# Optimization experiments

Measured on AMD Instinct MI355X. Metric: run time of the kernel, lower is better.

Reference implementation:

```python
import jax, jax.numpy as jnp
import numpy as np

B, S, H = 2, 2048, 2048
NH, NG = 16, 4           # attention heads, query groups
HD = H // NH             # head_dim = 128
HPG = NH // NG           # heads per group = 4


def setup_inputs() -> dict:
    key = jax.random.key(0)
    ks = jax.random.split(key, 8)
    s = 0.02
    return {
        "hidden_states": jax.random.normal(ks[0], (B, S, H), dtype=jnp.float32),
        "attention_mask": jnp.ones((B, S), dtype=jnp.int32),
        "Wq": jax.random.normal(ks[1], (H, H), dtype=jnp.float32) * s,
        "bq": jnp.zeros((H,), dtype=jnp.float32),
        "Wk": jax.random.normal(ks[2], (HD * NG, H), dtype=jnp.float32) * s,
        "bk": jnp.zeros((HD * NG,), dtype=jnp.float32),
        "Wv": jax.random.normal(ks[3], (HD * NG, H), dtype=jnp.float32) * s,
        "bv": jnp.zeros((HD * NG,), dtype=jnp.float32),
    }


def reference(hidden_states, attention_mask, Wq, bq, Wk, bk, Wv, bv):
    b, s, _ = hidden_states.shape
    scale = 1.0 / np.sqrt(HD).astype(np.float32)
    # projections (torch Linear: x @ W.T + b)
    q = hidden_states @ Wq.T + bq                      # [b,s,H]
    k = hidden_states @ Wk.T + bk                      # [b,s,NG*HD]
    v = hidden_states @ Wv.T + bv
    # q grouped so that repeat_interleave of k/v along heads == broadcast over heads_per_group
    q = q.reshape(b, s, NG, HPG, HD)                   # heads = group-major order
    k = k.reshape(b, s, NG, HD)
    v = v.reshape(b, s, NG, HD)
    scores = jnp.einsum("bsgpd,btgd->bgpst", q, k) * scale  # [b,NG,HPG,s,s]
    # mask: positions with attention_mask == 0 get finfo.min added
    mask_add = jnp.where(attention_mask == 0,
                         jnp.finfo(scores.dtype).min,
                         jnp.float32(0.0))             # [b,t]
    scores = scores + mask_add[:, None, None, None, :]
    attn = jax.nn.softmax(scores, axis=-1)             # dropout is identity in eval
    out = jnp.einsum("bgpst,btgd->bsgpd", attn, v)     # [b,s,NG,HPG,HD]
    return out.reshape(b, s, NH * HD)
```

## Files before the change

### kernel.cpp

```cpp
#include <hip/hip_runtime.h>
#include <hip/hip_bf16.h>

#define B_ 2
#define S_ 2048
#define H_ 2048
#define NH_ 16
#define NG_ 4
#define HD_ 128
#define HPG_ 4

typedef __attribute__((ext_vector_type(8))) short short8;
typedef __attribute__((ext_vector_type(4))) short short4v;
typedef __attribute__((ext_vector_type(4))) float float4v;

#define MFMA_BF16 __builtin_amdgcn_mfma_f32_16x16x32_bf16

#if __has_builtin(__builtin_amdgcn_exp2f)
#define EXP2(x) __builtin_amdgcn_exp2f(x)
#else
#define EXP2(x) exp2f(x)
#endif

__device__ __forceinline__ void gload16(const void* g, void* l) {
    __builtin_amdgcn_global_load_lds(
        (const __attribute__((address_space(1))) unsigned int*)g,
        (__attribute__((address_space(3))) unsigned int*)l, 16, 0, 0);
}

__device__ __forceinline__ short bf16bits(float f) {
    union { __hip_bfloat16 h; short s; } u;
    u.h = __float2bfloat16(f);
    return u.s;
}

__global__ __launch_bounds__(256) void cvt_all(const float* __restrict__ hs,
                                               const float* __restrict__ wq,
                                               const float* __restrict__ wk,
                                               const float* __restrict__ wv,
                                               const int* __restrict__ mask,
                                               __hip_bfloat16* __restrict__ o_hs,
                                               __hip_bfloat16* __restrict__ o_wq,
                                               __hip_bfloat16* __restrict__ o_wk,
                                               __hip_bfloat16* __restrict__ o_wv,
                                               float* __restrict__ o_m) {
    int i = blockIdx.x * 256 + threadIdx.x;
    if (blockIdx.x == 0) {
#pragma unroll
        for (int j = 0; j < 16; ++j) {
            int idx = threadIdx.x * 16 + j;
            o_m[idx] = mask[idx] ? 0.0f : -3.0e38f;
        }
    }
    const float* src;
    __hip_bfloat16* dst;
    int off;
    if (i < 1048576)      { src = hs; dst = o_hs; off = i; }
    else if (i < 1572864) { src = wq; dst = o_wq; off = i - 1048576; }
    else if (i < 1703936) { src = wk; dst = o_wk; off = i - 1572864; }
    else                  { src = wv; dst = o_wv; off = i - 1703936; }
    const float4* s4 = (const float4*)src;
    float4 a = s4[2 * (size_t)off];
    float4 b = s4[2 * (size_t)off + 1];
    union { short8 s; __hip_bfloat16 h[8]; } u;
    u.h[0] = __float2bfloat16(a.x); u.h[1] = __float2bfloat16(a.y);
    u.h[2] = __float2bfloat16(a.z); u.h[3] = __float2bfloat16(a.w);
    u.h[4] = __float2bfloat16(b.x); u.h[5] = __float2bfloat16(b.y);
    u.h[6] = __float2bfloat16(b.z); u.h[7] = __float2bfloat16(b.w);
    *(short8*)(dst + 8 * (size_t)off) = u.s;
}

__global__ __launch_bounds__(256) void gemm_qkv(const __hip_bfloat16* __restrict__ A,
                                                const __hip_bfloat16* __restrict__ Wq,
                                                const __hip_bfloat16* __restrict__ Wk,
                                                const __hip_bfloat16* __restrict__ Wv,
                                                const float* __restrict__ bq,
                                                const float* __restrict__ bk,
                                                const float* __restrict__ bv,
                                                __hip_bfloat16* __restrict__ qO,
                                                __hip_bfloat16* __restrict__ kO,
                                                __hip_bfloat16* __restrict__ vTO) {
    __shared__ char lds[32768];

    const int bx = blockIdx.x;
    const __hip_bfloat16* Bw;
    const float* bias;
    int bn, mode;
    if (bx < 16)      { Bw = Wq; bias = bq; bn = bx * 128;        mode = 0; }
    else if (bx < 20) { Bw = Wk; bias = bk; bn = (bx - 16) * 128; mode = 1; }
    else              { Bw = Wv; bias = bv; bn = (bx - 20) * 128; mode = 2; }

    const int tid = threadIdx.x;
    const int lane = tid & 63;
    const int x = lane & 15, g = lane >> 4;
    const int wid = tid >> 6;
    const int wm = wid >> 1, wn = wid & 1;
    const int bm = blockIdx.y * 128;
    const int K = 2048;

    const int srow = tid >> 2;
    const int schunk = (tid & 3) ^ ((tid >> 3) & 3);
    const __hip_bfloat16* gA0 = A + (size_t)(bm + srow) * K + schunk * 8;
    const __hip_bfloat16* gA1 = A + (size_t)(bm + 64 + srow) * K + schunk * 8;
    const __hip_bfloat16* gB0 = Bw + (size_t)(bn + srow) * K + schunk * 8;
    const __hip_bfloat16* gB1 = Bw + (size_t)(bn + 64 + srow) * K + schunk * 8;

    int aoff[4], boff[4];
    const int key = (x >> 1) & 3;
#pragma unroll
    for (int t = 0; t < 4; ++t) {
        aoff[t] = ((wm * 64 + t * 16 + x) * 32 + (g ^ key) * 8) * 2;
        boff[t] = 8192 + ((wn * 64 + t * 16 + x) * 32 + (g ^ key) * 8) * 2;
    }

    float4v acc[4][4];
#pragma unroll
    for (int i = 0; i < 4; ++i)
#pragma unroll
        for (int j = 0; j < 4; ++j) acc[i][j] = (float4v)0.f;

    gload16(gA0, lds + tid * 16);
    gload16(gA1, lds + tid * 16 + 4096);
    gload16(gB0, lds + 8192 + tid * 16);
    gload16(gB1, lds + 8192 + tid * 16 + 4096);
    gA0 += 32; gA1 += 32; gB0 += 32; gB1 += 32;

    for (int it = 0; it < 64; ++it) {
        char* cur = lds + (it & 1) * 16384;
        char* nxt = lds + ((it & 1) ^ 1) * 16384;
        __syncthreads();
        if (it < 63) {
            gload16(gA0, nxt + tid * 16);
            gload16(gA1, nxt + tid * 16 + 4096);
            gload16(gB0, nxt + 8192 + tid * 16);
            gload16(gB1, nxt + 8192 + tid * 16 + 4096);
            gA0 += 32; gA1 += 32; gB0 += 32; gB1 += 32;
        }
        short8 af[4], bf[4];
#pragma unroll
        for (int t = 0; t < 4; ++t) {
            af[t] = *(const short8*)(cur + aoff[t]);
            bf[t] = *(const short8*)(cur + boff[t]);
        }
#pragma unroll
        for (int mb = 0; mb < 4; ++mb)
#pragma unroll
            for (int nb = 0; nb < 4; ++nb)
                acc[mb][nb] = MFMA_BF16(af[mb], bf[nb], acc[mb][nb], 0, 0, 0);
    }

    if (mode <= 1) {
        const int N = (mode == 0) ? 2048 : 512;
        __hip_bfloat16* C = (mode == 0) ? qO : kO;
#pragma unroll
        for (int nb = 0; nb < 4; ++nb) {
            const int n = bn + wn * 64 + nb * 16 + x;
            const float bsv = bias[n];
#pragma unroll
            for (int mb = 0; mb < 4; ++mb) {
                const int m0 = bm + wm * 64 + mb * 16 + g * 4;
#pragma unroll
                for (int r = 0; r < 4; ++r)
                    C[(size_t)(m0 + r) * N + n] = __float2bfloat16(acc[mb][nb][r] + bsv);
            }
        }
    } else {
#pragma unroll
        for (int nb = 0; nb < 4; ++nb) {
            const int n = bn + wn * 64 + nb * 16 + x;
            const float bsv = bias[n];
            const int gv = n >> 7, d = n & 127;
#pragma unroll
            for (int mb = 0; mb < 4; ++mb) {
                const int m0 = bm + wm * 64 + mb * 16 + g * 4;
                const int bb = m0 >> 11, s = m0 & 2047;
                short4v pk;
#pragma unroll
                for (int r = 0; r < 4; ++r) pk[r] = bf16bits(acc[mb][nb][r] + bsv);
                *(short4v*)(vTO + ((size_t)(bb * NG_ + gv) * HD_ + d) * S_ + s) = pk;
            }
        }
    }
}

__global__ __launch_bounds__(256, 2) void attn(const __hip_bfloat16* __restrict__ q,
                                               const __hip_bfloat16* __restrict__ k,
                                               const __hip_bfloat16* __restrict__ vT,
                                               const float* __restrict__ M,
                                               float* __restrict__ out) {
    __shared__ char smem[50176];
    char* Ks = smem;
    char* Vs = smem + 16384;
    char* Ps = smem + 32768;

    const int tid = threadIdx.x;
    const int lane = tid & 63;
    const int w = tid >> 6;
    const int wm = w >> 1, wn = w & 1;
    const int x = lane & 15, g = lane >> 4;

    const int bid = blockIdx.x;
    const int qt = bid & 15;
    const int hp = (bid >> 4) & 3;
    const int gi = (bid >> 6) & 3;
    const int b = bid >> 8;
    const int head = gi * HPG_ + hp;
    const int q0 = qt * 128;

    short8 qf[4][4];
#pragma unroll
    for (int nb = 0; nb < 4; ++nb) {
        const int qq = q0 + wn * 64 + nb * 16 + x;
        const __hip_bfloat16* qrow = q + ((size_t)(b * S_ + qq) * NH_ + head) * HD_ + g * 8;
#pragma unroll
        for (int ks = 0; ks < 4; ++ks)
            qf[nb][ks] = *(const short8*)(qrow + ks * 32);
    }

    const int krow = tid >> 4;
    const int kchunk = (tid & 15) ^ krow;
    const __hip_bfloat16* kp = k + ((size_t)(b * S_ + krow) * NG_ + gi) * HD_ + kchunk * 8;
    const int vrow = tid >> 3;
    const int vchunk = (tid & 7) ^ (vrow & 7);
    const __hip_bfloat16* vp = vT + ((size_t)(b * NG_ + gi) * HD_ + vrow) * S_ + vchunk * 8;
    const float* mp = M + b * S_ + wm * 32 + g * 4;

    float4v O[4][4];
#pragma unroll
    for (int i = 0; i < 4; ++i)
#pragma unroll
        for (int j = 0; j < 4; ++j) O[i][j] = (float4v)0.f;
    float l_part[4] = {0.f, 0.f, 0.f, 0.f};

    const float SM = 0.08838834764831845f * 1.4426950408889634f;

#pragma unroll
    for (int qq = 0; qq < 4; ++qq)
        gload16(kp + qq * 8192, Ks + tid * 16 + qq * 4096);
    kp += 32768;

    for (int it = 0; it < 32; ++it) {
        __syncthreads();
        float4 mv0 = *(const float4*)(mp);
        float4 mv1 = *(const float4*)(mp + 16);
        mp += 64;
#pragma unroll
        for (int qq = 0; qq < 4; ++qq)
            gload16(vp + (size_t)qq * 65536, Vs + tid * 16 + qq * 4096);
        vp += 64;

        float4v sc[2][4];
#pragma unroll
        for (int i = 0; i < 2; ++i)
#pragma unroll
            for (int j = 0; j < 4; ++j) sc[i][j] = (float4v)0.f;
#pragma unroll
        for (int ks = 0; ks < 4; ++ks) {
            short8 af0 = *(const short8*)(Ks + (wm * 32 + x) * 256 + (((ks * 4 + g) ^ x) * 16));
            short8 af1 = *(const short8*)(Ks + (wm * 32 + 16 + x) * 256 + (((ks * 4 + g) ^ x) * 16));
#pragma unroll
            for (int nb = 0; nb < 4; ++nb) {
                sc[0][nb] = MFMA_BF16(af0, qf[nb][ks], sc[0][nb], 0, 0, 0);
                sc[1][nb] = MFMA_BF16(af1, qf[nb][ks], sc[1][nb], 0, 0, 0);
            }
        }

#pragma unroll
        for (int mb = 0; mb < 2; ++mb) {
            const float4 mv = mb ? mv1 : mv0;
            const int hs = wm * 8 + mb * 4 + g;
#pragma unroll
            for (int nb = 0; nb < 4; ++nb) {
                float p0 = EXP2(fmaf(sc[mb][nb][0], SM, mv.x));
                float p1 = EXP2(fmaf(sc[mb][nb][1], SM, mv.y));
                float p2 = EXP2(fmaf(sc[mb][nb][2], SM, mv.z));
                float p3 = EXP2(fmaf(sc[mb][nb][3], SM, mv.w));
                l_part[nb] += (p0 + p1) + (p2 + p3);
                short4v pk;
                pk[0] = bf16bits(p0); pk[1] = bf16bits(p1);
                pk[2] = bf16bits(p2); pk[3] = bf16bits(p3);
                *(short4v*)(Ps + (wn * 64 + nb * 16 + x) * 136 + hs * 8) = pk;
            }
        }

        __syncthreads();
        if (it < 31) {
#pragma unroll
            for (int qq = 0; qq < 4; ++qq)
                gload16(kp + qq * 8192, Ks + tid * 16 + qq * 4096);
            kp += 32768;
        }

#pragma unroll
        for (int ks = 0; ks < 2; ++ks) {
            short8 vf[4], pf[4];
#pragma unroll
            for (int i4 = 0; i4 < 4; ++i4) {
                vf[i4] = *(const short8*)(Vs + (wm * 64 + i4 * 16 + x) * 128 +
                                          (((ks * 4 + g) ^ (x & 7)) * 16));
                const char* pb = Ps + (wn * 64 + i4 * 16 + x) * 136 + (8 * ks + 2 * g) * 8;
                union { short4v h[2]; short8 s8; } uu;
                uu.h[0] = *(const short4v*)pb;
                uu.h[1] = *(const short4v*)(pb + 8);
                pf[i4] = uu.s8;
            }
#pragma unroll
            for (int mb = 0; mb < 4; ++mb)
#pragma unroll
                for (int nb = 0; nb < 4; ++nb)
                    O[mb][nb] = MFMA_BF16(vf[mb], pf[nb], O[mb][nb], 0, 0, 0);
        }
    }

    __syncthreads();
#pragma unroll
    for (int nb = 0; nb < 4; ++nb) {
        l_part[nb] += __shfl_xor(l_part[nb], 16);
        l_part[nb] += __shfl_xor(l_part[nb], 32);
    }
    float* lws = (float*)Ps;
    if (g == 0) {
#pragma unroll
        for (int nb = 0; nb < 4; ++nb)
            lws[wm * 128 + wn * 64 + nb * 16 + x] = l_part[nb];
    }
    __syncthreads();
    float inv[4];
#pragma unroll
    for (int nb = 0; nb < 4; ++nb)
        inv[nb] = 1.0f / (l_part[nb] + lws[(wm ^ 1) * 128 + wn * 64 + nb * 16 + x]);

#pragma unroll
    for (int mb = 0; mb < 4; ++mb) {
#pragma unroll
        for (int nb = 0; nb < 4; ++nb) {
            const int qq = q0 + wn * 64 + nb * 16 + x;
            const int d0 = wm * 64 + mb * 16 + g * 4;
            float4v o = O[mb][nb] * inv[nb];
            *(float4v*)(out + (size_t)(b * S_ + qq) * H_ + head * HD_ + d0) = o;
        }
    }
}

extern "C" void kernel_launch(void* const* d_in, const int* in_sizes, int n_in,
                              void* d_out, int out_size, void* d_ws, size_t ws_size,
                              hipStream_t stream) {
    (void)in_sizes; (void)n_in; (void)out_size; (void)ws_size;
    const float* hs = (const float*)d_in[0];
    const int* amask = (const int*)d_in[1];
    const float* Wq = (const float*)d_in[2];
    const float* bq = (const float*)d_in[3];
    const float* Wk = (const float*)d_in[4];
    const float* bk = (const float*)d_in[5];
    const float* Wv = (const float*)d_in[6];
    const float* bv = (const float*)d_in[7];
    float* out = (float*)d_out;

    char* ws = (char*)d_ws;
    __hip_bfloat16* hsB = (__hip_bfloat16*)(ws);
    __hip_bfloat16* WqB = (__hip_bfloat16*)(ws + 16777216);
    __hip_bfloat16* WkB = (__hip_bfloat16*)(ws + 25165824);
    __hip_bfloat16* WvB = (__hip_bfloat16*)(ws + 27262976);
    __hip_bfloat16* qB  = (__hip_bfloat16*)(ws + 29360128);
    __hip_bfloat16* kB  = (__hip_bfloat16*)(ws + 46137344);
    __hip_bfloat16* vTB = (__hip_bfloat16*)(ws + 50331648);
    float* Mf           = (float*)(ws + 54525952);

    cvt_all<<<7168, 256, 0, stream>>>(hs, Wq, Wk, Wv, amask, hsB, WqB, WkB, WvB, Mf);
    gemm_qkv<<<dim3(24, 32), 256, 0, stream>>>(hsB, WqB, WkB, WvB, bq, bk, bv, qB, kB, vTB);
    attn<<<512, 256, 0, stream>>>(qB, kB, vTB, Mf, out);
}
```

Before: 249.0 us.

## Triple-buffer QKV GEMM loads and double-buffer K with swizzled P in attention

The QKV projection GEMM moves from a double-buffered to a triple-buffered LDS pipeline. It waits on partial vmcnt plus a raw barrier instead of a full __syncthreads, so two tiles stay in flight. The attention kernel double-buffers K tiles so the next K load is issued at the top of the iteration, and replaces __syncthreads with vmcnt/lgkmcnt waits plus barriers. It also changes the P tile layout from a padded 136-byte stride to an XOR-swizzled 128-byte stride, so P fragments load as single 16-byte reads. The cost is more LDS per block: 64KB for attention, which may reduce occupancy below two blocks per CU, and hand-written waitcnt counts that must match the issued loads.

```diff
diff --git a/kernel.cpp b/kernel.cpp
--- a/kernel.cpp
+++ b/kernel.cpp
@@ -79,7 +79,7 @@
                                                 __hip_bfloat16* __restrict__ qO,
                                                 __hip_bfloat16* __restrict__ kO,
                                                 __hip_bfloat16* __restrict__ vTO) {
-    __shared__ char lds[32768];
+    __shared__ char lds[49152];
 
     const int bx = blockIdx.x;
     const __hip_bfloat16* Bw;
@@ -118,34 +118,47 @@
 #pragma unroll
         for (int j = 0; j < 4; ++j) acc[i][j] = (float4v)0.f;
 
-    gload16(gA0, lds + tid * 16);
-    gload16(gA1, lds + tid * 16 + 4096);
-    gload16(gB0, lds + 8192 + tid * 16);
-    gload16(gB1, lds + 8192 + tid * 16 + 4096);
+    char* s0 = lds;
+    char* s1 = lds + 16384;
+    char* s2 = lds + 32768;
+
+    gload16(gA0, s0 + tid * 16);
+    gload16(gA1, s0 + tid * 16 + 4096);
+    gload16(gB0, s0 + 8192 + tid * 16);
+    gload16(gB1, s0 + 8192 + tid * 16 + 4096);
     gA0 += 32; gA1 += 32; gB0 += 32; gB1 += 32;
+    gload16(gA0, s1 + tid * 16);
+    gload16(gA1, s1 + tid * 16 + 4096);
+    gload16(gB0, s1 + 8192 + tid * 16);
+    gload16(gB1, s1 + 8192 + tid * 16 + 4096);
+    gA0 += 32; gA1 += 32; gB0 += 32; gB1 += 32;
 
     for (int it = 0; it < 64; ++it) {
-        char* cur = lds + (it & 1) * 16384;
-        char* nxt = lds + ((it & 1) ^ 1) * 16384;
-        __syncthreads();
         if (it < 63) {
-            gload16(gA0, nxt + tid * 16);
-            gload16(gA1, nxt + tid * 16 + 4096);
-            gload16(gB0, nxt + 8192 + tid * 16);
-            gload16(gB1, nxt + 8192 + tid * 16 + 4096);
+            asm volatile("s_waitcnt vmcnt(4)" ::: "memory");
+        } else {
+            asm volatile("s_waitcnt vmcnt(0)" ::: "memory");
+        }
+        __builtin_amdgcn_s_barrier();
+        if (it < 62) {
+            gload16(gA0, s2 + tid * 16);
+            gload16(gA1, s2 + tid * 16 + 4096);
+            gload16(gB0, s2 + 8192 + tid * 16);
+            gload16(gB1, s2 + 8192 + tid * 16 + 4096);
             gA0 += 32; gA1 += 32; gB0 += 32; gB1 += 32;
         }
         short8 af[4], bf[4];
 #pragma unroll
         for (int t = 0; t < 4; ++t) {
-            af[t] = *(const short8*)(cur + aoff[t]);
-            bf[t] = *(const short8*)(cur + boff[t]);
+            af[t] = *(const short8*)(s0 + aoff[t]);
+            bf[t] = *(const short8*)(s0 + boff[t]);
         }
 #pragma unroll
         for (int mb = 0; mb < 4; ++mb)
 #pragma unroll
             for (int nb = 0; nb < 4; ++nb)
                 acc[mb][nb] = MFMA_BF16(af[mb], bf[nb], acc[mb][nb], 0, 0, 0);
+        char* tswp = s0; s0 = s1; s1 = s2; s2 = tswp;
     }
 
     if (mode <= 1) {
@@ -187,10 +200,11 @@
                                                const __hip_bfloat16* __restrict__ vT,
                                                const float* __restrict__ M,
                                                float* __restrict__ out) {
-    __shared__ char smem[50176];
-    char* Ks = smem;
-    char* Vs = smem + 16384;
-    char* Ps = smem + 32768;
+    __shared__ char smem[65536];
+    char* Kb0 = smem;
+    char* Kb1 = smem + 16384;
+    char* Vs  = smem + 32768;
+    char* Ps  = smem + 49152;
 
     const int tid = threadIdx.x;
     const int lane = tid & 63;
@@ -232,14 +246,18 @@
     float l_part[4] = {0.f, 0.f, 0.f, 0.f};
 
     const float SM = 0.08838834764831845f * 1.4426950408889634f;
+    const int pkey = x & 14;
 
 #pragma unroll
     for (int qq = 0; qq < 4; ++qq)
-        gload16(kp + qq * 8192, Ks + tid * 16 + qq * 4096);
+        gload16(kp + qq * 8192, Kb0 + tid * 16 + qq * 4096);
     kp += 32768;
 
     for (int it = 0; it < 32; ++it) {
-        __syncthreads();
+        char* Kc = (it & 1) ? Kb1 : Kb0;
+        char* Kn = (it & 1) ? Kb0 : Kb1;
+        asm volatile("s_waitcnt vmcnt(0)" ::: "memory");
+        __builtin_amdgcn_s_barrier();
         float4 mv0 = *(const float4*)(mp);
         float4 mv1 = *(const float4*)(mp + 16);
         mp += 64;
@@ -247,6 +265,12 @@
         for (int qq = 0; qq < 4; ++qq)
             gload16(vp + (size_t)qq * 65536, Vs + tid * 16 + qq * 4096);
         vp += 64;
+        if (it < 31) {
+#pragma unroll
+            for (int qq = 0; qq < 4; ++qq)
+                gload16(kp + qq * 8192, Kn + tid * 16 + qq * 4096);
+            kp += 32768;
+        }
 
         float4v sc[2][4];
 #pragma unroll
@@ -255,8 +279,8 @@
             for (int j = 0; j < 4; ++j) sc[i][j] = (float4v)0.f;
 #pragma unroll
         for (int ks = 0; ks < 4; ++ks) {
-            short8 af0 = *(const short8*)(Ks + (wm * 32 + x) * 256 + (((ks * 4 + g) ^ x) * 16));
-            short8 af1 = *(const short8*)(Ks + (wm * 32 + 16 + x) * 256 + (((ks * 4 + g) ^ x) * 16));
+            short8 af0 = *(const short8*)(Kc + (wm * 32 + x) * 256 + (((ks * 4 + g) ^ x) * 16));
+            short8 af1 = *(const short8*)(Kc + (wm * 32 + 16 + x) * 256 + (((ks * 4 + g) ^ x) * 16));
 #pragma unroll
             for (int nb = 0; nb < 4; ++nb) {
                 sc[0][nb] = MFMA_BF16(af0, qf[nb][ks], sc[0][nb], 0, 0, 0);
@@ -278,17 +302,16 @@
                 short4v pk;
                 pk[0] = bf16bits(p0); pk[1] = bf16bits(p1);
                 pk[2] = bf16bits(p2); pk[3] = bf16bits(p3);
-                *(short4v*)(Ps + (wn * 64 + nb * 16 + x) * 136 + hs * 8) = pk;
-            }
-        }
-
-        __syncthreads();
+                *(short4v*)(Ps + (wn * 64 + nb * 16 + x) * 128 + ((hs ^ pkey) * 8)) = pk;
+            }
+        }
+
         if (it < 31) {
-#pragma unroll
-            for (int qq = 0; qq < 4; ++qq)
-                gload16(kp + qq * 8192, Ks + tid * 16 + qq * 4096);
-            kp += 32768;
-        }
+            asm volatile("s_waitcnt vmcnt(4) lgkmcnt(0)" ::: "memory");
+        } else {
+            asm volatile("s_waitcnt vmcnt(0) lgkmcnt(0)" ::: "memory");
+        }
+        __builtin_amdgcn_s_barrier();
 
 #pragma unroll
         for (int ks = 0; ks < 2; ++ks) {
@@ -297,11 +320,8 @@
             for (int i4 = 0; i4 < 4; ++i4) {
                 vf[i4] = *(const short8*)(Vs + (wm * 64 + i4 * 16 + x) * 128 +
                                           (((ks * 4 + g) ^ (x & 7)) * 16));
-                const char* pb = Ps + (wn * 64 + i4 * 16 + x) * 136 + (8 * ks + 2 * g) * 8;
-                union { short4v h[2]; short8 s8; } uu;
-                uu.h[0] = *(const short4v*)pb;
-                uu.h[1] = *(const short4v*)(pb + 8);
-                pf[i4] = uu.s8;
+                pf[i4] = *(const short8*)(Ps + (wn * 64 + i4 * 16 + x) * 128 +
+                                          (((8 * ks + 2 * g) ^ pkey) * 8));
             }
 #pragma unroll
             for (int mb = 0; mb < 4; ++mb)
```

Result: no change. 253.4 us (+1.8%).

## Double-buffer K tiles in attention and XOR-swizzle the P buffer

Applied to the files above, without the earlier changes.

Splits K shared storage into two ping-pong buffers so the next K tile load is issued at the top of each iteration and overlaps with the QK and PV compute, instead of being issued after the mid-iteration barrier. Replaces __syncthreads with explicit vmcnt/lgkmcnt waits plus s_barrier so the prefetched K loads can stay in flight. Also changes the P staging buffer from a padded 136-byte stride to a 128-byte stride with an XOR swizzle to avoid LDS bank conflicts. Shared memory grows to 64 KB per block, which may limit how many blocks fit on a CU alongside launch_bounds(256,2).

```diff
diff --git a/kernel.cpp b/kernel.cpp
--- a/kernel.cpp
+++ b/kernel.cpp
@@ -187,10 +187,11 @@
                                                const __hip_bfloat16* __restrict__ vT,
                                                const float* __restrict__ M,
                                                float* __restrict__ out) {
-    __shared__ char smem[50176];
-    char* Ks = smem;
-    char* Vs = smem + 16384;
-    char* Ps = smem + 32768;
+    __shared__ char smem[65536];
+    char* Kb0 = smem;
+    char* Kb1 = smem + 16384;
+    char* Vs  = smem + 32768;
+    char* Ps  = smem + 49152;
 
     const int tid = threadIdx.x;
     const int lane = tid & 63;
@@ -235,11 +236,14 @@
 
 #pragma unroll
     for (int qq = 0; qq < 4; ++qq)
-        gload16(kp + qq * 8192, Ks + tid * 16 + qq * 4096);
+        gload16(kp + qq * 8192, Kb0 + tid * 16 + qq * 4096);
     kp += 32768;
 
     for (int it = 0; it < 32; ++it) {
-        __syncthreads();
+        char* Kc = (it & 1) ? Kb1 : Kb0;
+        char* Kn = (it & 1) ? Kb0 : Kb1;
+        asm volatile("s_waitcnt vmcnt(0)" ::: "memory");
+        __builtin_amdgcn_s_barrier();
         float4 mv0 = *(const float4*)(mp);
         float4 mv1 = *(const float4*)(mp + 16);
         mp += 64;
@@ -247,6 +251,12 @@
         for (int qq = 0; qq < 4; ++qq)
             gload16(vp + (size_t)qq * 65536, Vs + tid * 16 + qq * 4096);
         vp += 64;
+        if (it < 31) {
+#pragma unroll
+            for (int qq = 0; qq < 4; ++qq)
+                gload16(kp + qq * 8192, Kn + tid * 16 + qq * 4096);
+            kp += 32768;
+        }
 
         float4v sc[2][4];
 #pragma unroll
@@ -255,8 +265,8 @@
             for (int j = 0; j < 4; ++j) sc[i][j] = (float4v)0.f;
 #pragma unroll
         for (int ks = 0; ks < 4; ++ks) {
-            short8 af0 = *(const short8*)(Ks + (wm * 32 + x) * 256 + (((ks * 4 + g) ^ x) * 16));
-            short8 af1 = *(const short8*)(Ks + (wm * 32 + 16 + x) * 256 + (((ks * 4 + g) ^ x) * 16));
+            short8 af0 = *(const short8*)(Kc + (wm * 32 + x) * 256 + (((ks * 4 + g) ^ x) * 16));
+            short8 af1 = *(const short8*)(Kc + (wm * 32 + 16 + x) * 256 + (((ks * 4 + g) ^ x) * 16));
 #pragma unroll
             for (int nb = 0; nb < 4; ++nb) {
                 sc[0][nb] = MFMA_BF16(af0, qf[nb][ks], sc[0][nb], 0, 0, 0);
@@ -278,29 +288,29 @@
                 short4v pk;
                 pk[0] = bf16bits(p0); pk[1] = bf16bits(p1);
                 pk[2] = bf16bits(p2); pk[3] = bf16bits(p3);
-                *(short4v*)(Ps + (wn * 64 + nb * 16 + x) * 136 + hs * 8) = pk;
-            }
-        }
-
-        __syncthreads();
+                *(short4v*)(Ps + (wn * 64 + nb * 16 + x) * 128 + ((hs ^ x) * 8)) = pk;
+            }
+        }
+
         if (it < 31) {
-#pragma unroll
-            for (int qq = 0; qq < 4; ++qq)
-                gload16(kp + qq * 8192, Ks + tid * 16 + qq * 4096);
-            kp += 32768;
-        }
+            asm volatile("s_waitcnt vmcnt(4) lgkmcnt(0)" ::: "memory");
+        } else {
+            asm volatile("s_waitcnt vmcnt(0) lgkmcnt(0)" ::: "memory");
+        }
+        __builtin_amdgcn_s_barrier();
 
 #pragma unroll
         for (int ks = 0; ks < 2; ++ks) {
             short8 vf[4], pf[4];
+            const int s0 = ks * 8 + 2 * g;
 #pragma unroll
             for (int i4 = 0; i4 < 4; ++i4) {
                 vf[i4] = *(const short8*)(Vs + (wm * 64 + i4 * 16 + x) * 128 +
                                           (((ks * 4 + g) ^ (x & 7)) * 16));
-                const char* pb = Ps + (wn * 64 + i4 * 16 + x) * 136 + (8 * ks + 2 * g) * 8;
+                const char* pb = Ps + (wn * 64 + i4 * 16 + x) * 128;
                 union { short4v h[2]; short8 s8; } uu;
-                uu.h[0] = *(const short4v*)pb;
-                uu.h[1] = *(const short4v*)(pb + 8);
+                uu.h[0] = *(const short4v*)(pb + ((s0 ^ x) * 8));
+                uu.h[1] = *(const short4v*)(pb + (((s0 + 1) ^ x) * 8));
                 pf[i4] = uu.s8;
             }
 #pragma unroll
```

Result: no change. 252.6 us (+1.5%).
